# Performance work log

Measured on AMD Instinct MI355X. Metric: run time of the kernel, lower is better.

The kernel has to match this reference:

```python
import jax, jax.numpy as jnp
import numpy as np

N_NODES = 100000
N_EDGES = 1600000
NEG_SLOPE = 0.2  # PyG GATConv default
BN_EPS = 1e-5


def gat_conv(x, src, dst, W, a_src, a_dst, bias):
    # x: [N, F], W: [F, H, C]
    h = jnp.einsum('nf,fhc->nhc', x, W)                 # [N, H, C]
    al_src = jnp.sum(h * a_src, axis=-1)                # [N, H]
    al_dst = jnp.sum(h * a_dst, axis=-1)                # [N, H]
    e = al_src[src] + al_dst[dst]                       # [E, H]
    e = jnp.where(e >= 0, e, NEG_SLOPE * e)             # leaky_relu(0.2)
    # segment softmax over incoming edges of each dst node
    emax = jax.ops.segment_max(e, dst, num_segments=N_NODES)
    ee = jnp.exp(e - emax[dst])
    denom = jax.ops.segment_sum(ee, dst, num_segments=N_NODES)
    alpha = ee / denom[dst]                             # [E, H]
    msg = alpha[:, :, None] * h[src]                    # [E, H, C]
    out = jax.ops.segment_sum(msg, dst, num_segments=N_NODES)  # [N, H, C]
    return out.mean(axis=1) + bias                      # concat=False -> head mean


def batch_norm(x, gamma, beta):
    mu = jnp.mean(x, axis=0)
    var = jnp.var(x, axis=0)  # biased, as in torch BN normalization
    return (x - mu) * jax.lax.rsqrt(var + BN_EPS) * gamma + beta


def setup_inputs() -> dict:
    key = jax.random.key(0)
    ks = jax.random.split(key, 16)
    inp = {
        'x': jax.random.normal(ks[0], (N_NODES, 128), jnp.float32),
        'edge_index': jax.random.randint(ks[1], (2, N_EDGES), 0, N_NODES, jnp.int64)
            if jax.config.jax_enable_x64 else
            jax.random.randint(ks[1], (2, N_EDGES), 0, N_NODES, jnp.int32),
        'edge_attr': jax.random.normal(ks[2], (N_EDGES, 8), jnp.float32),
        'W0': 0.1 * jax.random.normal(ks[3], (128, 4, 32), jnp.float32),
        'a_src0': 0.1 * jax.random.normal(ks[4], (4, 32), jnp.float32),
        'a_dst0': 0.1 * jax.random.normal(ks[5], (4, 32), jnp.float32),
        'b0': jnp.zeros((32,), jnp.float32),
        'g0': jnp.ones((32,), jnp.float32),
        'be0': jnp.zeros((32,), jnp.float32),
        'W1': 0.1 * jax.random.normal(ks[6], (32, 4, 32), jnp.float32),
        'a_src1': 0.1 * jax.random.normal(ks[7], (4, 32), jnp.float32),
        'a_dst1': 0.1 * jax.random.normal(ks[8], (4, 32), jnp.float32),
        'b1': jnp.zeros((32,), jnp.float32),
        'g1': jnp.ones((32,), jnp.float32),
        'be1': jnp.zeros((32,), jnp.float32),
        'W2': 0.1 * jax.random.normal(ks[9], (32, 4, 32), jnp.float32),
        'a_src2': 0.1 * jax.random.normal(ks[10], (4, 32), jnp.float32),
        'a_dst2': 0.1 * jax.random.normal(ks[11], (4, 32), jnp.float32),
        'b2': jnp.zeros((32,), jnp.float32),
    }
    return inp


def reference(x, edge_index, edge_attr, W0, a_src0, a_dst0, b0, g0, be0,
              W1, a_src1, a_dst1, b1, g1, be1, W2, a_src2, a_dst2, b2):
    src, dst = edge_index[0], edge_index[1]
    h = gat_conv(x, src, dst, W0, a_src0, a_dst0, b0)
    h = jax.nn.relu(batch_norm(h, g0, be0))  # dropout = identity (deterministic ref)
    h = gat_conv(h, src, dst, W1, a_src1, a_dst1, b1)
    h = jax.nn.relu(batch_norm(h, g1, be1))
    h = gat_conv(h, src, dst, W2, a_src2, a_dst2, b2)
    return (h, edge_attr)
```

## Files before the change

### kernel.cpp

```cpp
#include <hip/hip_runtime.h>
#include <cstdio>
#include <cstdint>

#define LRELU 0.2f
#define BN_EPS 1e-5f

typedef short bf16x8 __attribute__((ext_vector_type(8)));
typedef float f32x4 __attribute__((ext_vector_type(4)));

__device__ inline unsigned short f2bf(float f) {
  unsigned int u = __float_as_uint(f);
  u += 0x7fffu + ((u >> 16) & 1u);
  return (unsigned short)(u >> 16);
}
__device__ inline float bf2f(unsigned short v) {
  return __uint_as_float(((unsigned int)v) << 16);
}
__device__ inline float bflo(unsigned int u) { return __uint_as_float(u << 16); }
__device__ inline float bfhi(unsigned int u) { return __uint_as_float(u & 0xffff0000u); }


__global__ __launch_bounds__(256) void k_bhist_cast_copy(
    const int* __restrict__ dst, int* __restrict__ bh, int E,
    const float* __restrict__ W0, const float* __restrict__ W1,
    const float* __restrict__ W2,
    unsigned short* __restrict__ Wt0, unsigned short* __restrict__ Wt1,
    unsigned short* __restrict__ Wt2,
    const f32x4* __restrict__ ea, f32x4* __restrict__ oea) {
  __shared__ int cnt[512];
  const int gid = blockIdx.x * blockDim.x + threadIdx.x;
  const int gstride = gridDim.x * blockDim.x;
  if (gid < 24576) {
    int o = gid;
    if (o < 16384) {
      int n = o >> 7, k = o & 127;
      Wt0[o] = f2bf(W0[k * 128 + n]);
    } else if (o < 20480) {
      int p = o - 16384, n = p >> 5, k = p & 31;
      Wt1[p] = f2bf(W1[k * 128 + n]);
    } else {
      int p = o - 20480, n = p >> 5, k = p & 31;
      Wt2[p] = f2bf(W2[k * 128 + n]);
    }
  }
  for (int b = threadIdx.x; b < 512; b += 256) cnt[b] = 0;
  __syncthreads();
  for (int i = gid; i < E; i += gstride) atomicAdd(&cnt[dst[i] >> 8], 1);
  const int n4 = E * 2;
  for (int i = gid; i < n4; i += gstride) {
    f32x4 v = __builtin_nontemporal_load(&ea[i]);
    __builtin_nontemporal_store(v, &oea[i]);
  }
  __syncthreads();
  for (int b = threadIdx.x; b < 512; b += 256)
    if (cnt[b]) atomicAdd(&bh[b], cnt[b]);
}

__device__ inline void scan_bh(const int* __restrict__ bh, int* pre, int* bsc) {
  const int t = threadIdx.x;
  const int a0 = bh[2 * t];
  const int a1 = bh[2 * t + 1];
  int s = a0 + a1;
  pre[t] = s;
  __syncthreads();
  for (int st = 1; st < 256; st <<= 1) {
    int u = (t >= st) ? pre[t - st] : 0;
    __syncthreads();
    pre[t] += u;
    __syncthreads();
  }
  const int ex = pre[t] - s;
  bsc[2 * t] = ex;
  bsc[2 * t + 1] = ex + a0;
  if (t == 255) bsc[512] = pre[255];
  __syncthreads();
}

__global__ __launch_bounds__(256) void k_bscatter(const int* __restrict__ src,
                                                  const int* __restrict__ dst,
                                                  const int* __restrict__ bh,
                                                  int* __restrict__ bclaim,
                                                  unsigned int* __restrict__ bpair,
                                                  int E) {
  __shared__ int pre[256];
  __shared__ int bsc[513];
  __shared__ int cnt[512];
  scan_bh(bh, pre, bsc);
  const int chunk = (E + gridDim.x - 1) / gridDim.x;
  const int beg = blockIdx.x * chunk;
  const int end = min(E, beg + chunk);
  for (int b = threadIdx.x; b < 512; b += 256) cnt[b] = 0;
  __syncthreads();
  for (int e = beg + threadIdx.x; e < end; e += 256)
    atomicAdd(&cnt[dst[e] >> 8], 1);
  __syncthreads();
  for (int b = threadIdx.x; b < 512; b += 256) {
    int c = cnt[b];
    cnt[b] = (c > 0) ? (bsc[b] + atomicAdd(&bclaim[b], c)) : 0;
  }
  __syncthreads();
  for (int e = beg + threadIdx.x; e < end; e += 256) {
    int d = dst[e];
    int pos = atomicAdd(&cnt[d >> 8], 1);
    bpair[pos] = ((unsigned)src[e] << 8) | ((unsigned)d & 255u);
  }
}

__global__ __launch_bounds__(256) void k_bcsr(const unsigned int* __restrict__ bpair,
                                              const int* __restrict__ bh,
                                              int* __restrict__ offs,
                                              int* __restrict__ srcs, int N, int E) {
  __shared__ int pre[256];
  __shared__ int bsc[513];
  __shared__ int sc[256];
  __shared__ int cur[256];
  scan_bh(bh, pre, bsc);
  const int b = blockIdx.x;
  const int lo = b << 8;
  const int t = threadIdx.x;
  const int e0 = bsc[b], e1 = bsc[b + 1];
  sc[t] = 0;
  __syncthreads();
  for (int e = e0 + t; e < e1; e += 256) atomicAdd(&sc[bpair[e] & 255u], 1);
  __syncthreads();
  int v = sc[t];
  for (int s = 1; s < 256; s <<= 1) {
    int u = (t >= s) ? sc[t - s] : 0;
    __syncthreads();
    sc[t] += u;
    __syncthreads();
  }
  const int pos0 = e0 + sc[t] - v;
  cur[t] = pos0;
  if (lo + t < N) offs[lo + t] = pos0;
  if (b == 0 && t == 0) offs[N] = E;
  __syncthreads();
  for (int e = e0 + t; e < e1; e += 256) {
    unsigned int p = bpair[e];
    int pos = atomicAdd(&cur[p & 255u], 1);
    srcs[pos] = (int)(p >> 8);
  }
}

template <int K, bool BN>
__global__ __launch_bounds__(256) void k_mfma(
    const float* __restrict__ Ain, const unsigned short* __restrict__ Wt,
    const float* __restrict__ asrc, const float* __restrict__ adst,
    const float* __restrict__ stats, const float* __restrict__ g,
    const float* __restrict__ be,
    unsigned short* __restrict__ h, float* __restrict__ als,
    float* __restrict__ ald, int N) {
  __shared__ unsigned short lsh[4][16 * 132];
  __shared__ float sc_s[32], sh_s[32];
  const int wv   = threadIdx.x >> 6;
  const int lane = threadIdx.x & 63;
  const int quad = lane >> 4;
  const int col  = lane & 15;
  const int m0   = blockIdx.x * 128 + wv * 16;
  const int m1   = m0 + 64;
  const int rowc0 = min(m0 + col, N - 1);
  const int rowc1 = min(m1 + col, N - 1);

  if constexpr (BN) {
    if (threadIdx.x < 32) {
      float s = 0.f, ss = 0.f;
#pragma unroll
      for (int r = 0; r < 8; r++) {
        s  += stats[r * 64 + threadIdx.x];
        ss += stats[r * 64 + 32 + threadIdx.x];
      }
      const float inv = 1.f / (float)N;
      const float mu = s * inv;
      const float var = ss * inv - mu * mu;
      const float scv = g[threadIdx.x] * rsqrtf(var + BN_EPS);
      sc_s[threadIdx.x] = scv;
      sh_s[threadIdx.x] = be[threadIdx.x] - mu * scv;
    }
    __syncthreads();
  }

  f32x4 acc0[8], acc1[8];
#pragma unroll
  for (int t = 0; t < 8; t++) {
    acc0[t] = (f32x4){0.f, 0.f, 0.f, 0.f};
    acc1[t] = (f32x4){0.f, 0.f, 0.f, 0.f};
  }

#pragma unroll
  for (int ks = 0; ks < K / 32; ks++) {
    const int k0 = ks * 32 + quad * 8;
    const float* ap0 = Ain + (size_t)rowc0 * K + k0;
    const float* ap1 = Ain + (size_t)rowc1 * K + k0;
    float4 f0 = *(const float4*)ap0;
    float4 f1 = *(const float4*)(ap0 + 4);
    float4 e0 = *(const float4*)ap1;
    float4 e1 = *(const float4*)(ap1 + 4);
    if constexpr (BN) {
      const float s0 = sc_s[k0 + 0], h0 = sh_s[k0 + 0];
      const float s1 = sc_s[k0 + 1], h1 = sh_s[k0 + 1];
      const float s2 = sc_s[k0 + 2], h2 = sh_s[k0 + 2];
      const float s3 = sc_s[k0 + 3], h3 = sh_s[k0 + 3];
      const float s4 = sc_s[k0 + 4], h4 = sh_s[k0 + 4];
      const float s5 = sc_s[k0 + 5], h5 = sh_s[k0 + 5];
      const float s6 = sc_s[k0 + 6], h6 = sh_s[k0 + 6];
      const float s7 = sc_s[k0 + 7], h7 = sh_s[k0 + 7];
      f0.x = fmaxf(0.f, fmaf(f0.x, s0, h0)); e0.x = fmaxf(0.f, fmaf(e0.x, s0, h0));
      f0.y = fmaxf(0.f, fmaf(f0.y, s1, h1)); e0.y = fmaxf(0.f, fmaf(e0.y, s1, h1));
      f0.z = fmaxf(0.f, fmaf(f0.z, s2, h2)); e0.z = fmaxf(0.f, fmaf(e0.z, s2, h2));
      f0.w = fmaxf(0.f, fmaf(f0.w, s3, h3)); e0.w = fmaxf(0.f, fmaf(e0.w, s3, h3));
      f1.x = fmaxf(0.f, fmaf(f1.x, s4, h4)); e1.x = fmaxf(0.f, fmaf(e1.x, s4, h4));
      f1.y = fmaxf(0.f, fmaf(f1.y, s5, h5)); e1.y = fmaxf(0.f, fmaf(e1.y, s5, h5));
      f1.z = fmaxf(0.f, fmaf(f1.z, s6, h6)); e1.z = fmaxf(0.f, fmaf(e1.z, s6, h6));
      f1.w = fmaxf(0.f, fmaf(f1.w, s7, h7)); e1.w = fmaxf(0.f, fmaf(e1.w, s7, h7));
    }
    bf16x8 a0, a1;
    a0[0] = (short)f2bf(f0.x); a0[1] = (short)f2bf(f0.y);
    a0[2] = (short)f2bf(f0.z); a0[3] = (short)f2bf(f0.w);
    a0[4] = (short)f2bf(f1.x); a0[5] = (short)f2bf(f1.y);
    a0[6] = (short)f2bf(f1.z); a0[7] = (short)f2bf(f1.w);
    a1[0] = (short)f2bf(e0.x); a1[1] = (short)f2bf(e0.y);
    a1[2] = (short)f2bf(e0.z); a1[3] = (short)f2bf(e0.w);
    a1[4] = (short)f2bf(e1.x); a1[5] = (short)f2bf(e1.y);
    a1[6] = (short)f2bf(e1.z); a1[7] = (short)f2bf(e1.w);
#pragma unroll
    for (int t = 0; t < 8; t++) {
      bf16x8 b = *(const bf16x8*)(Wt + (size_t)(t * 16 + col) * K + k0);
      acc0[t] = __builtin_amdgcn_mfma_f32_16x16x32_bf16(a0, b, acc0[t], 0, 0, 0);
      acc1[t] = __builtin_amdgcn_mfma_f32_16x16x32_bf16(a1, b, acc1[t], 0, 0, 0);
    }
  }

  float as8[8], ad8[8];
#pragma unroll
  for (int j = 0; j < 8; j++) {
    as8[j] = asrc[col * 8 + j];
    ad8[j] = adst[col * 8 + j];
  }

#define EPILOGUE(MM, ACC)                                                    \
  {                                                                          \
    _Pragma("unroll") for (int t = 0; t < 8; t++) {                          \
      _Pragma("unroll") for (int j = 0; j < 4; j++)                          \
          lsh[wv][(quad * 4 + j) * 132 + col + 16 * t] = f2bf(ACC[t][j]);    \
    }                                                                        \
    _Pragma("unroll") for (int i = 0; i < 4; i++) {                          \
      const int row = i * 4 + quad;                                          \
      const int hrow = (MM) + row;                                           \
      const unsigned short* rp = &lsh[wv][row * 132 + col * 8];              \
      ushort4 lo = *(const ushort4*)rp;                                      \
      ushort4 hi = *(const ushort4*)(rp + 4);                                \
      float p = 0.f, q = 0.f, v;                                             \
      v = bf2f(lo.x); p += v * as8[0]; q += v * ad8[0];                      \
      v = bf2f(lo.y); p += v * as8[1]; q += v * ad8[1];                      \
      v = bf2f(lo.z); p += v * as8[2]; q += v * ad8[2];                      \
      v = bf2f(lo.w); p += v * as8[3]; q += v * ad8[3];                      \
      v = bf2f(hi.x); p += v * as8[4]; q += v * ad8[4];                      \
      v = bf2f(hi.y); p += v * as8[5]; q += v * ad8[5];                      \
      v = bf2f(hi.z); p += v * as8[6]; q += v * ad8[6];                      \
      v = bf2f(hi.w); p += v * as8[7]; q += v * ad8[7];                      \
      if (hrow < N) {                                                        \
        ushort4* gp = (ushort4*)(h + (size_t)hrow * 128 + col * 8);          \
        gp[0] = lo; gp[1] = hi;                                              \
      }                                                                      \
      p += __shfl_xor(p, 1); p += __shfl_xor(p, 2);                          \
      q += __shfl_xor(q, 1); q += __shfl_xor(q, 2);                          \
      if ((lane & 3) == 0 && hrow < N) {                                     \
        const int head = col >> 2;                                           \
        als[hrow * 4 + head] = p;                                            \
        ald[hrow * 4 + head] = q;                                            \
      }                                                                      \
    }                                                                        \
  }

  EPILOGUE(m0, acc0)
  EPILOGUE(m1, acc1)
#undef EPILOGUE
}

template <bool STATS>
__global__ __launch_bounds__(256) void k_agg(
    const unsigned int* __restrict__ h2, const float* __restrict__ als,
    const float* __restrict__ ald, const int* __restrict__ offs,
    const int* __restrict__ srcs, const float* __restrict__ bias,
    float* __restrict__ y, float* __restrict__ stats, int N) {
  __shared__ float s1[32], s2[32];
  const int node = blockIdx.x * 4 + (threadIdx.x >> 6);
  const int lane = threadIdx.x & 63;
  const bool valid = node < N;
  if constexpr (STATS) {
    if (threadIdx.x < 32) { s1[threadIdx.x] = 0.f; s2[threadIdx.x] = 0.f; }
    __syncthreads();
  } else {
    if (!valid) return;
  }

  if (valid) {
    const int half = lane >> 5;
    const int sub  = lane & 31;
    const int head = sub >> 3;
    const int beg = __builtin_amdgcn_readfirstlane(offs[node]);
    const int end = __builtin_amdgcn_readfirstlane(offs[node + 1]);
    const float ad = ald[node * 4 + head];
    float ax0 = 0.f, ax1 = 0.f, ax2 = 0.f, ax3 = 0.f, dn = 0.f;

    for (int base = beg; base < end; base += 64) {
      const int mm = min(64, end - base);
      const int sv = srcs[base + min(lane, mm - 1)];
      const int vlim = mm - half;

      float aA0, aA1, aA2, aA3, aB0, aB1, aB2, aB3;
      uint2 uA0, uA1, uA2, uA3, uB0, uB1, uB2, uB3;
      int iA0, iA1, iA2, iA3, iB0, iB1, iB2, iB3;

#define SLOT(S, K, I)                                                      \
  {                                                                        \
    i##S##K = (I);                                                         \
    const int c0 = min((I), mm - 1), c1 = min((I) + 1, mm - 1);            \
    const int sA_ = __builtin_amdgcn_readlane(sv, c0);                     \
    const int sB_ = __builtin_amdgcn_readlane(sv, c1);                     \
    const int s_ = half ? sB_ : sA_;                                       \
    a##S##K = als[s_ * 4 + head];                                          \
    u##S##K = *(const uint2*)(h2 + (size_t)s_ * 64 + (sub << 1));          \
  }
#define ISSUE(S, J0) SLOT(S, 0, (J0)) SLOT(S, 1, (J0) + 2)                 \
                     SLOT(S, 2, (J0) + 4) SLOT(S, 3, (J0) + 6)
#define CSLOT(S, K)                                                        \
  {                                                                        \
    float e_ = a##S##K + ad;                                               \
    e_ = fmaxf(e_, LRELU * e_);                                            \
    float w_ = __expf(e_);                                                 \
    w_ = (i##S##K < vlim) ? w_ : 0.f;                                      \
    dn += w_;                                                              \
    ax0 = fmaf(w_, bflo(u##S##K.x), ax0);                                  \
    ax1 = fmaf(w_, bfhi(u##S##K.x), ax1);                                  \
    ax2 = fmaf(w_, bflo(u##S##K.y), ax2);                                  \
    ax3 = fmaf(w_, bfhi(u##S##K.y), ax3);                                  \
  }
#define COMPUTE(S) CSLOT(S, 0) CSLOT(S, 1) CSLOT(S, 2) CSLOT(S, 3)

      int j0 = 0;
      ISSUE(A, 0)
      j0 = 8;
      if (j0 >= mm) {
        COMPUTE(A)
      } else {
        for (;;) {
          ISSUE(B, j0) COMPUTE(A)
          j0 += 8;
          if (j0 >= mm) { COMPUTE(B) break; }
          ISSUE(A, j0) COMPUTE(B)
          j0 += 8;
          if (j0 >= mm) { COMPUTE(A) break; }
        }
      }
#undef SLOT
#undef ISSUE
#undef CSLOT
#undef COMPUTE
    }

    dn += __shfl_xor(dn, 32);
    const float r = (dn > 0.f) ? (1.f / dn) : 0.f;
    ax0 *= r; ax1 *= r; ax2 *= r; ax3 *= r;
    ax0 += __shfl_xor(ax0, 32); ax1 += __shfl_xor(ax1, 32);
    ax2 += __shfl_xor(ax2, 32); ax3 += __shfl_xor(ax3, 32);
    ax0 += __shfl_xor(ax0, 8);  ax1 += __shfl_xor(ax1, 8);
    ax2 += __shfl_xor(ax2, 8);  ax3 += __shfl_xor(ax3, 8);
    ax0 += __shfl_xor(ax0, 16); ax1 += __shfl_xor(ax1, 16);
    ax2 += __shfl_xor(ax2, 16); ax3 += __shfl_xor(ax3, 16);

    if (lane < 8) {
      float4 b4 = ((const float4*)bias)[lane];
      float4 o;
      o.x = 0.25f * ax0 + b4.x;
      o.y = 0.25f * ax1 + b4.y;
      o.z = 0.25f * ax2 + b4.z;
      o.w = 0.25f * ax3 + b4.w;
      ((float4*)(y + (size_t)node * 32))[lane] = o;
      if constexpr (STATS) {
        atomicAdd(&s1[4 * lane + 0], o.x); atomicAdd(&s2[4 * lane + 0], o.x * o.x);
        atomicAdd(&s1[4 * lane + 1], o.y); atomicAdd(&s2[4 * lane + 1], o.y * o.y);
        atomicAdd(&s1[4 * lane + 2], o.z); atomicAdd(&s2[4 * lane + 2], o.z * o.z);
        atomicAdd(&s1[4 * lane + 3], o.w); atomicAdd(&s2[4 * lane + 3], o.w * o.w);
      }
    }
  }

  if constexpr (STATS) {
    __syncthreads();
    if (threadIdx.x < 32) {
      float* sb = stats + (blockIdx.x & 7) * 64;
      atomicAdd(&sb[threadIdx.x], s1[threadIdx.x]);
      atomicAdd(&sb[32 + threadIdx.x], s2[threadIdx.x]);
    }
  }
}

extern "C" void kernel_launch(void* const* d_in, const int* in_sizes, int n_in,
                              void* d_out, int out_size, void* d_ws, size_t ws_size,
                              hipStream_t stream) {
  const float* x   = (const float*)d_in[0];
  const int*   ei  = (const int*)d_in[1];
  const float* ea  = (const float*)d_in[2];
  const float* W0  = (const float*)d_in[3];
  const float* as0 = (const float*)d_in[4];
  const float* ad0 = (const float*)d_in[5];
  const float* b0  = (const float*)d_in[6];
  const float* g0  = (const float*)d_in[7];
  const float* be0 = (const float*)d_in[8];
  const float* W1  = (const float*)d_in[9];
  const float* as1 = (const float*)d_in[10];
  const float* ad1 = (const float*)d_in[11];
  const float* b1  = (const float*)d_in[12];
  const float* g1  = (const float*)d_in[13];
  const float* be1 = (const float*)d_in[14];
  const float* W2  = (const float*)d_in[15];
  const float* as2 = (const float*)d_in[16];
  const float* ad2 = (const float*)d_in[17];
  const float* b2  = (const float*)d_in[18];

  const int N = in_sizes[0] / 128;
  const int E = in_sizes[1] / 2;
  const int* srcI = ei;
  const int* dstI = ei + E;
  const int NB = (N + 255) >> 8;

  char* w = (char*)d_ws;
  auto carve = [&](size_t bytes) -> void* {
    void* p = (void*)w;
    w += (bytes + 255) & ~(size_t)255;
    return p;
  };
  unsigned short* h  = (unsigned short*)carve((size_t)N * 128 * 2);
  float* als        = (float*)carve((size_t)N * 4 * 4);
  float* ald        = (float*)carve((size_t)N * 4 * 4);
  float* y          = (float*)carve((size_t)N * 32 * 4);
  int* offs         = (int*)carve((size_t)(N + 1) * 4);
  int* srcs         = (int*)carve((size_t)E * 4);
  int* bh           = (int*)carve(512 * 4);
  int* bclaim       = (int*)carve(512 * 4);
  float* stats      = (float*)carve(1024 * 4);
  char* zend        = w;
  unsigned short* Wt0 = (unsigned short*)carve(128 * 128 * 2);
  unsigned short* Wt1 = (unsigned short*)carve(128 * 32 * 2);
  unsigned short* Wt2 = (unsigned short*)carve(128 * 32 * 2);
  if ((size_t)(w - (char*)d_ws) > ws_size) {
    fprintf(stderr, "GAT kernel: ws too small (%zu needed, %zu given)\n",
            (size_t)(w - (char*)d_ws), ws_size);
    return;
  }
  unsigned int* bpair = (unsigned int*)h;

  float* out_nodes = (float*)d_out;
  float* out_ea    = out_nodes + (size_t)N * 32;

  (void)hipMemsetAsync(bh, 0, (size_t)(zend - (char*)bh), stream);

  k_bhist_cast_copy<<<2048, 256, 0, stream>>>(dstI, bh, E, W0, W1, W2,
                                              Wt0, Wt1, Wt2,
                                              (const f32x4*)ea, (f32x4*)out_ea);
  k_bscatter<<<512, 256, 0, stream>>>(srcI, dstI, bh, bclaim, bpair, E);
  k_bcsr<<<NB, 256, 0, stream>>>(bpair, bh, offs, srcs, N, E);

  const int gGemm = (N + 127) / 128;
  const int gAgg  = (N + 3) / 4;

  k_mfma<128, false><<<gGemm, 256, 0, stream>>>(x, Wt0, as0, ad0,
                                                nullptr, nullptr, nullptr,
                                                h, als, ald, N);
  k_agg<true><<<gAgg, 256, 0, stream>>>((const unsigned int*)h, als, ald, offs,
                                        srcs, b0, y, stats, N);
  k_mfma<32, true><<<gGemm, 256, 0, stream>>>(y, Wt1, as1, ad1, stats, g0, be0,
                                              h, als, ald, N);
  k_agg<true><<<gAgg, 256, 0, stream>>>((const unsigned int*)h, als, ald, offs,
                                        srcs, b1, y, stats + 512, N);
  k_mfma<32, true><<<gGemm, 256, 0, stream>>>(y, Wt2, as2, ad2, stats + 512, g1, be1,
                                              h, als, ald, N);
  k_agg<false><<<gAgg, 256, 0, stream>>>((const unsigned int*)h, als, ald, offs,
                                         srcs, b2, out_nodes, nullptr, N);
}
```

Before: 580.9 us.

## Co-schedule edge bucketing with first GEMM and overlap edge_attr copy with last aggregation

Merges the bucket-scatter kernel and the layer-0 MFMA GEMM into one launch whose blocks are split by index, so the two independent stages can run concurrently. The edge_attr passthrough copy moves out of the histogram kernel into extra blocks of the final aggregation kernel, so bandwidth-bound copying overlaps the latency-bound gather. bpair gets its own workspace buffer because it can no longer alias h while the GEMM writes h. The histogram grid shrinks to 512 blocks. The merged kernel uses a larger shared-memory footprint, which may reduce occupancy for the scatter blocks.

```diff
diff --git a/kernel.cpp b/kernel.cpp
--- a/kernel.cpp
+++ b/kernel.cpp
@@ -20,13 +20,12 @@
 __device__ inline float bfhi(unsigned int u) { return __uint_as_float(u & 0xffff0000u); }
 
 
-__global__ __launch_bounds__(256) void k_bhist_cast_copy(
+__global__ __launch_bounds__(256) void k_bhist_cast(
     const int* __restrict__ dst, int* __restrict__ bh, int E,
     const float* __restrict__ W0, const float* __restrict__ W1,
     const float* __restrict__ W2,
     unsigned short* __restrict__ Wt0, unsigned short* __restrict__ Wt1,
-    unsigned short* __restrict__ Wt2,
-    const f32x4* __restrict__ ea, f32x4* __restrict__ oea) {
+    unsigned short* __restrict__ Wt2) {
   __shared__ int cnt[512];
   const int gid = blockIdx.x * blockDim.x + threadIdx.x;
   const int gstride = gridDim.x * blockDim.x;
@@ -46,17 +45,13 @@
   for (int b = threadIdx.x; b < 512; b += 256) cnt[b] = 0;
   __syncthreads();
   for (int i = gid; i < E; i += gstride) atomicAdd(&cnt[dst[i] >> 8], 1);
-  const int n4 = E * 2;
-  for (int i = gid; i < n4; i += gstride) {
-    f32x4 v = __builtin_nontemporal_load(&ea[i]);
-    __builtin_nontemporal_store(v, &oea[i]);
-  }
   __syncthreads();
   for (int b = threadIdx.x; b < 512; b += 256)
     if (cnt[b]) atomicAdd(&bh[b], cnt[b]);
 }
 
-__device__ inline void scan_bh(const int* __restrict__ bh, int* pre, int* bsc) {
+__device__ __forceinline__ void scan_bh(const int* __restrict__ bh, int* pre,
+                                        int* bsc) {
   const int t = threadIdx.x;
   const int a0 = bh[2 * t];
   const int a1 = bh[2 * t + 1];
@@ -76,18 +71,14 @@
   __syncthreads();
 }
 
-__global__ __launch_bounds__(256) void k_bscatter(const int* __restrict__ src,
-                                                  const int* __restrict__ dst,
-                                                  const int* __restrict__ bh,
-                                                  int* __restrict__ bclaim,
-                                                  unsigned int* __restrict__ bpair,
-                                                  int E) {
-  __shared__ int pre[256];
-  __shared__ int bsc[513];
-  __shared__ int cnt[512];
+__device__ __forceinline__ void bscatter_body(
+    int bid, int SCB, int* pre, int* bsc, int* cnt,
+    const int* __restrict__ src, const int* __restrict__ dst,
+    const int* __restrict__ bh, int* __restrict__ bclaim,
+    unsigned int* __restrict__ bpair, int E) {
   scan_bh(bh, pre, bsc);
-  const int chunk = (E + gridDim.x - 1) / gridDim.x;
-  const int beg = blockIdx.x * chunk;
+  const int chunk = (E + SCB - 1) / SCB;
+  const int beg = bid * chunk;
   const int end = min(E, beg + chunk);
   for (int b = threadIdx.x; b < 512; b += 256) cnt[b] = 0;
   __syncthreads();
@@ -143,20 +134,19 @@
 }
 
 template <int K, bool BN>
-__global__ __launch_bounds__(256) void k_mfma(
+__device__ __forceinline__ void mfma_body(
+    int bid, unsigned short (*lsh)[2112], float* sc_s, float* sh_s,
     const float* __restrict__ Ain, const unsigned short* __restrict__ Wt,
     const float* __restrict__ asrc, const float* __restrict__ adst,
     const float* __restrict__ stats, const float* __restrict__ g,
     const float* __restrict__ be,
     unsigned short* __restrict__ h, float* __restrict__ als,
     float* __restrict__ ald, int N) {
-  __shared__ unsigned short lsh[4][16 * 132];
-  __shared__ float sc_s[32], sh_s[32];
   const int wv   = threadIdx.x >> 6;
   const int lane = threadIdx.x & 63;
   const int quad = lane >> 4;
   const int col  = lane & 15;
-  const int m0   = blockIdx.x * 128 + wv * 16;
+  const int m0   = bid * 128 + wv * 16;
   const int m1   = m0 + 64;
   const int rowc0 = min(m0 + col, N - 1);
   const int rowc1 = min(m1 + col, N - 1);
@@ -277,12 +267,60 @@
 #undef EPILOGUE
 }
 
-template <bool STATS>
+template <int K, bool BN>
+__global__ __launch_bounds__(256) void k_mfma(
+    const float* __restrict__ Ain, const unsigned short* __restrict__ Wt,
+    const float* __restrict__ asrc, const float* __restrict__ adst,
+    const float* __restrict__ stats, const float* __restrict__ g,
+    const float* __restrict__ be,
+    unsigned short* __restrict__ h, float* __restrict__ als,
+    float* __restrict__ ald, int N) {
+  __shared__ unsigned short lsh[4][2112];
+  __shared__ float sc_s[32], sh_s[32];
+  mfma_body<K, BN>(blockIdx.x, lsh, sc_s, sh_s, Ain, Wt, asrc, adst,
+                   stats, g, be, h, als, ald, N);
+}
+
+__global__ __launch_bounds__(256) void k_sc_mfma(
+    const int* __restrict__ src, const int* __restrict__ dst,
+    const int* __restrict__ bh, int* __restrict__ bclaim,
+    unsigned int* __restrict__ bpair, int E, int SCB,
+    const float* __restrict__ Ain, const unsigned short* __restrict__ Wt,
+    const float* __restrict__ asrc, const float* __restrict__ adst,
+    unsigned short* __restrict__ h, float* __restrict__ als,
+    float* __restrict__ ald, int N) {
+  __shared__ __align__(16) char smraw[16896];
+  if ((int)blockIdx.x < SCB) {
+    int* pre = (int*)smraw;
+    int* bsc = pre + 256;
+    int* cnt = bsc + 513;
+    bscatter_body(blockIdx.x, SCB, pre, bsc, cnt, src, dst, bh, bclaim,
+                  bpair, E);
+  } else {
+    unsigned short (*lsh)[2112] = (unsigned short(*)[2112])smraw;
+    mfma_body<128, false>(blockIdx.x - SCB, lsh, nullptr, nullptr, Ain, Wt,
+                          asrc, adst, nullptr, nullptr, nullptr, h, als, ald, N);
+  }
+}
+
+template <bool STATS, bool COPY>
 __global__ __launch_bounds__(256) void k_agg(
     const unsigned int* __restrict__ h2, const float* __restrict__ als,
     const float* __restrict__ ald, const int* __restrict__ offs,
     const int* __restrict__ srcs, const float* __restrict__ bias,
-    float* __restrict__ y, float* __restrict__ stats, int N) {
+    float* __restrict__ y, float* __restrict__ stats, int N,
+    int aggBlocks, const f32x4* __restrict__ cs, f32x4* __restrict__ cd,
+    int cn) {
+  if constexpr (COPY) {
+    if ((int)blockIdx.x >= aggBlocks) {
+      const int cb = blockIdx.x - aggBlocks;
+      for (int i = cb * 256 + threadIdx.x; i < cn; i += 1024 * 256) {
+        f32x4 v = __builtin_nontemporal_load(&cs[i]);
+        __builtin_nontemporal_store(v, &cd[i]);
+      }
+      return;
+    }
+  }
   __shared__ float s1[32], s2[32];
   const int node = blockIdx.x * 4 + (threadIdx.x >> 6);
   const int lane = threadIdx.x & 63;
@@ -437,6 +475,7 @@
   float* y          = (float*)carve((size_t)N * 32 * 4);
   int* offs         = (int*)carve((size_t)(N + 1) * 4);
   int* srcs         = (int*)carve((size_t)E * 4);
+  unsigned int* bpair = (unsigned int*)carve((size_t)E * 4);
   int* bh           = (int*)carve(512 * 4);
   int* bclaim       = (int*)carve(512 * 4);
   float* stats      = (float*)carve(1024 * 4);
@@ -449,33 +488,35 @@
             (size_t)(w - (char*)d_ws), ws_size);
     return;
   }
-  unsigned int* bpair = (unsigned int*)h;
 
   float* out_nodes = (float*)d_out;
   float* out_ea    = out_nodes + (size_t)N * 32;
 
   (void)hipMemsetAsync(bh, 0, (size_t)(zend - (char*)bh), stream);
 
-  k_bhist_cast_copy<<<2048, 256, 0, stream>>>(dstI, bh, E, W0, W1, W2,
-                                              Wt0, Wt1, Wt2,
-                                              (const f32x4*)ea, (f32x4*)out_ea);
-  k_bscatter<<<512, 256, 0, stream>>>(srcI, dstI, bh, bclaim, bpair, E);
-  k_bcsr<<<NB, 256, 0, stream>>>(bpair, bh, offs, srcs, N, E);
+  k_bhist_cast<<<512, 256, 0, stream>>>(dstI, bh, E, W0, W1, W2, Wt0, Wt1, Wt2);
 
   const int gGemm = (N + 127) / 128;
   const int gAgg  = (N + 3) / 4;
-
-  k_mfma<128, false><<<gGemm, 256, 0, stream>>>(x, Wt0, as0, ad0,
-                                                nullptr, nullptr, nullptr,
-                                                h, als, ald, N);
-  k_agg<true><<<gAgg, 256, 0, stream>>>((const unsigned int*)h, als, ald, offs,
-                                        srcs, b0, y, stats, N);
+  const int SCB   = 512;
+  const int n4    = E * 2;
+
+  k_sc_mfma<<<SCB + gGemm, 256, 0, stream>>>(srcI, dstI, bh, bclaim, bpair, E,
+                                             SCB, x, Wt0, as0, ad0,
+                                             h, als, ald, N);
+  k_bcsr<<<NB, 256, 0, stream>>>(bpair, bh, offs, srcs, N, E);
+
+  k_agg<true, false><<<gAgg, 256, 0, stream>>>(
+      (const unsigned int*)h, als, ald, offs, srcs, b0, y, stats, N,
+      0, nullptr, nullptr, 0);
   k_mfma<32, true><<<gGemm, 256, 0, stream>>>(y, Wt1, as1, ad1, stats, g0, be0,
                                               h, als, ald, N);
-  k_agg<true><<<gAgg, 256, 0, stream>>>((const unsigned int*)h, als, ald, offs,
-                                        srcs, b1, y, stats + 512, N);
+  k_agg<true, false><<<gAgg, 256, 0, stream>>>(
+      (const unsigned int*)h, als, ald, offs, srcs, b1, y, stats + 512, N,
+      0, nullptr, nullptr, 0);
   k_mfma<32, true><<<gGemm, 256, 0, stream>>>(y, Wt2, as2, ad2, stats + 512, g1, be1,
                                               h, als, ald, N);
-  k_agg<false><<<gAgg, 256, 0, stream>>>((const unsigned int*)h, als, ald, offs,
-                                         srcs, b2, out_nodes, nullptr, N);
-}
+  k_agg<false, true><<<gAgg + 1024, 256, 0, stream>>>(
+      (const unsigned int*)h, als, ald, offs, srcs, b2, out_nodes, nullptr, N,
+      gAgg, (const f32x4*)ea, (f32x4*)out_ea, n4);
+}
```

Result: faster. 544.3 us (-6.3%).
